# Optimization experiments

Hardware: AMD Instinct MI355X
Metric: run time of the kernel (lower is better)

## Reference

```python
import jax, jax.numpy as jnp
import numpy as np

IN_DIM, HIDDEN, OUT_DIM, BRANCH = 700, 1024, 20, 4
B, T = 128, 250
VTH = 1.0
WARMUP = 0
# surrogate-gradient constants (DH-SNN ActFun_adp); only used in backward
GAMMA, LENS, SCALE, HIGHT = 0.5, 0.5, 6.0, 0.15
SQRT2PI = float(np.sqrt(2.0 * np.pi))


def _gauss(x, mu, sigma):
    return jnp.exp(-((x - mu) ** 2) / (2.0 * sigma * sigma)) / (SQRT2PI * sigma)


@jax.custom_vjp
def spike_fn(x):
    # heaviside spike with multi-gaussian surrogate gradient
    return (x > 0).astype(x.dtype)


def _spike_fwd(x):
    return spike_fn(x), x


def _spike_bwd(x, g):
    temp = (_gauss(x, 0.0, LENS) * (1.0 + HIGHT)
            - _gauss(x, LENS, SCALE * LENS) * HIGHT
            - _gauss(x, -LENS, SCALE * LENS) * HIGHT)
    return (g * temp * GAMMA,)


spike_fn.defvjp(_spike_fwd, _spike_bwd)


def _branch_mask(rng):
    # each neuron's branch j sees a random disjoint slice of the (input+recurrent) fan-in
    isz = IN_DIM + HIDDEN
    seg = isz // BRANCH
    mask = np.zeros((HIDDEN * BRANCH, isz), np.float32)
    for i in range(HIDDEN):
        perm = rng.permutation(isz)
        for j in range(BRANCH):
            mask[i * BRANCH + j, perm[j * seg:(j + 1) * seg]] = 1.0
    return mask


def setup_inputs() -> dict:
    key = jax.random.key(0)
    ks = jax.random.split(key, 8)
    isz = IN_DIM + HIDDEN
    x = jax.random.normal(ks[0], (B, T, IN_DIM), jnp.float32)
    W = jax.random.normal(ks[1], (HIDDEN * BRANCH, isz), jnp.float32) / np.float32(np.sqrt(isz))
    W = W * jnp.asarray(_branch_mask(np.random.RandomState(0)))  # apply_mask() pre-applied
    b = jnp.zeros((HIDDEN * BRANCH,), jnp.float32)
    tau_m = jax.random.uniform(ks[2], (HIDDEN,), jnp.float32, 0.0, 4.0)
    tau_n = jax.random.uniform(ks[3], (HIDDEN, BRANCH), jnp.float32, 2.0, 6.0)  # low_n/high_n
    Wr = jax.random.normal(ks[4], (OUT_DIM, HIDDEN), jnp.float32) / np.float32(np.sqrt(HIDDEN))
    br = jnp.zeros((OUT_DIM,), jnp.float32)
    tau_r = jax.random.uniform(ks[5], (OUT_DIM,), jnp.float32, 0.0, 4.0)
    mem0 = jax.random.uniform(ks[6], (B, HIDDEN), jnp.float32) * VTH  # set_neuron_state: rand*vth
    return {"x": x, "W": W, "b": b, "tau_m": tau_m, "tau_n": tau_n,
            "Wr": Wr, "br": br, "tau_r": tau_r, "mem0": mem0}


def reference(x, W, b, tau_m, tau_n, Wr, br, tau_r, mem0):
    Bsz, Tlen = x.shape[0], x.shape[1]
    beta = jax.nn.sigmoid(tau_n)      # [H, BR] dendritic branch decay
    alpha = jax.nn.sigmoid(tau_m)     # [H]     soma decay
    alpha_r = jax.nn.sigmoid(tau_r)   # [O]     readout decay
    spike0 = jnp.zeros((Bsz, HIDDEN), x.dtype)
    d0 = jnp.zeros((Bsz, HIDDEN, BRANCH), x.dtype)
    rmem0 = jnp.zeros((Bsz, OUT_DIM), x.dtype)
    acc0 = jnp.zeros((Bsz, OUT_DIM), x.dtype)

    def step(carry, inp):
        mem, spk, d_in, rmem, acc = carry
        x_t, t = inp
        k = jnp.concatenate([x_t, spk], axis=1)                 # [B, in+H]
        cur = (k @ W.T + b).reshape(Bsz, HIDDEN, BRANCH)        # branch currents
        d_in = beta * d_in + (1.0 - beta) * cur                 # dendritic integration
        l_in = d_in.sum(axis=2)                                 # [B, H]
        mem = mem * alpha + (1.0 - alpha) * l_in - VTH * spk    # soma, soft reset (R_m=1)
        spk = spike_fn(mem - VTH)
        rmem = rmem * alpha_r + (1.0 - alpha_r) * (spk @ Wr.T + br)
        acc = acc + jnp.where(t > WARMUP, jax.nn.softmax(rmem, axis=1), 0.0)
        return (mem, spk, d_in, rmem, acc), None

    xs = (jnp.swapaxes(x, 0, 1), jnp.arange(Tlen))
    (_, _, _, _, acc), _ = jax.lax.scan(step, (mem0, spike0, d0, rmem0, acc0), xs)
    return acc
```

## Files before the change

### kernel.cpp

```cpp
#include <hip/hip_runtime.h>
#include <hip/hip_bf16.h>
#include <stdint.h>


typedef short short8 __attribute__((ext_vector_type(8)));
typedef float f32x4 __attribute__((ext_vector_type(4)));

#define T_STEPS 250
#define BATCH   128
#define HID     1024
#define NCOL    4096
#define IND     700
#define ISZ     1724
#define KPAD    704
#define OUTD    20
#define WGT     256
#define UPB     5632

#define O_P1F   0
#define O_SUM   4096
#define O_CHK   8192
#define O_WST   73728
#define O_WXH   16850944
#define O_XH    22618112

#define SM_BP    0
#define SM_A2    45568
#define SM_CURL2 135680
#define SM_MTB   144896
#define SM_TOTAL 153600

#define AGENT __HIP_MEMORY_SCOPE_AGENT

__device__ __forceinline__ float sigmoidf(float x) { return 1.0f / (1.0f + expf(-x)); }

__device__ __forceinline__ unsigned ldsLd(const unsigned* p) {
    return __hip_atomic_load(p, __ATOMIC_ACQUIRE, __HIP_MEMORY_SCOPE_WORKGROUP);
}
__device__ __forceinline__ void ldsSt(unsigned* p, unsigned v) {
    __hip_atomic_store(p, v, __ATOMIC_RELEASE, __HIP_MEMORY_SCOPE_WORKGROUP);
}

__device__ __forceinline__ void dma16(const void* g, void* l) {
    __builtin_amdgcn_global_load_lds(
        (const __attribute__((address_space(1))) unsigned int*)g,
        (__attribute__((address_space(3))) unsigned int*)l, 16, 0, 0);
}

__device__ __forceinline__ float qsum4(float v) {
    union { float f; int i; } a, b;
    a.f = v; b.i = __builtin_amdgcn_mov_dpp(a.i, 0xB1, 0xF, 0xF, true); v += b.f;
    a.f = v; b.i = __builtin_amdgcn_mov_dpp(a.i, 0x4E, 0xF, 0xF, true); v += b.f;
    return v;
}

__global__ void prep_x(const float* __restrict__ x, __hip_bfloat16* __restrict__ Xh) {
    const int total = T_STEPS * 2 * UPB;
    for (int unit = blockIdx.x * blockDim.x + threadIdx.x; unit < total;
         unit += gridDim.x * blockDim.x) {
        int q   = unit % UPB;
        int blk = unit / UPB;
        int half = blk & 1, t = blk >> 1;
        int row = q / 88, m = q % 88;
        int k8  = m ^ (row & 7);
        int b   = half * 64 + row;
        const float* xp = x + ((long)b * T_STEPS + t) * IND + k8 * 8;
        short8 o;
        #pragma unroll
        for (int e = 0; e < 8; ++e) {
            int k = k8 * 8 + e;
            float v = (k < IND) ? xp[e] : 0.0f;
            union { __hip_bfloat16 h; short s; } u;
            u.h = __float2bfloat16(v);
            o[e] = u.s;
        }
        *(short8*)(Xh + (size_t)unit * 8) = o;
    }
}

__global__ void prep_w(const float* __restrict__ W, __hip_bfloat16* __restrict__ Wxh,
                       uint64_t* __restrict__ p1f, uint64_t* __restrict__ sums,
                       uint64_t* __restrict__ chunks) {
    if (blockIdx.x == 0) {
        for (int i = threadIdx.x; i < 512; i += blockDim.x)
            __hip_atomic_store(&p1f[i], 0ull, __ATOMIC_RELAXED, AGENT);
        for (int i = threadIdx.x; i < 2 * 2 * 128; i += blockDim.x)
            __hip_atomic_store(&sums[i], 0ull, __ATOMIC_RELAXED, AGENT);
        for (int i = threadIdx.x; i < 2 * 2 * 128 * 16; i += blockDim.x)
            __hip_atomic_store(&chunks[i], 0ull, __ATOMIC_RELAXED, AGENT);
    }
    const int total = NCOL * KPAD;
    for (int idx = blockIdx.x * blockDim.x + threadIdx.x; idx < total; idx += gridDim.x * blockDim.x) {
        int k = idx % KPAD;
        int n = idx / KPAD;
        float v = (k < IND) ? W[(long)n * ISZ + k] : 0.0f;
        Wxh[idx] = __float2bfloat16(v);
    }
}

__global__ __launch_bounds__(256) void prep_t(const float* __restrict__ W, float* __restrict__ Wst) {
    __shared__ float tile[32][33];
    const int h0 = blockIdx.x * 32, n0 = blockIdx.y * 32;
    const int tx = threadIdx.x, ty = threadIdx.y;
    #pragma unroll
    for (int j = 0; j < 32; j += 8)
        tile[ty + j][tx] = W[(long)(n0 + ty + j) * ISZ + IND + h0 + tx];
    __syncthreads();
    #pragma unroll
    for (int j = 0; j < 32; j += 8)
        Wst[(long)(h0 + ty + j) * NCOL + n0 + tx] = tile[tx][ty + j];
}

__global__ __launch_bounds__(256, 2) void p1_scan(
    const __hip_bfloat16* __restrict__ Xh, const __hip_bfloat16* __restrict__ Wxh,
    const float* __restrict__ bvec, const float* __restrict__ tau_m,
    const float* __restrict__ tau_n, const float* __restrict__ mem0,
    uint64_t* __restrict__ p1f)
{
    __shared__ __align__(16) uint8_t Abuf[3 * 22528];
    __shared__ __align__(16) float preg[8 * 256];
    __shared__ unsigned anySpkF;

    const int wg    = blockIdx.x;
    const int rtile = wg & 7;
    const int ctile = wg >> 3;
    const int tid   = threadIdx.x;
    const int lane  = tid & 63, wid = tid >> 6;
    const int colA  = lane & 15, kb8 = (lane >> 4) * 8;
    const int cg    = wid >> 1;
    const int p     = wid & 1;

    if (tid == 0) anySpkF = 0u;

    const int colG0 = ctile * 64 + cg * 32 + colA;
    const int colG1 = colG0 + 16;
    const int rowB  = rtile * 16 + (lane >> 4) * 4;
    float bt_[2], omb_[2], bias_[2], al_[2], oma_[2], dn[2][4], mem_[2][4];
    {
        const int cG[2] = {colG0, colG1};
        #pragma unroll
        for (int i = 0; i < 2; ++i) {
            bt_[i]   = sigmoidf(tau_n[cG[i]]);
            omb_[i]  = 1.0f - bt_[i];
            bias_[i] = bvec[cG[i]];
            al_[i]   = sigmoidf(tau_m[cG[i] >> 2]);
            oma_[i]  = 1.0f - al_[i];
            #pragma unroll
            for (int j = 0; j < 4; ++j) {
                dn[i][j]   = 0.0f;
                mem_[i][j] = mem0[(rowB + j) * HID + (cG[i] >> 2)];
            }
        }
    }

    short8 Breg[22];
    #pragma unroll
    for (int j = 0; j < 11; ++j) {
        Breg[2 * j]     = *(const short8*)(Wxh + (long)colG0 * KPAD + (11 * p + j) * 32 + kb8);
        Breg[2 * j + 1] = *(const short8*)(Wxh + (long)colG1 * KPAD + (11 * p + j) * 32 + kb8);
    }
    asm volatile("s_waitcnt vmcnt(0)" ::: "memory");
    __builtin_amdgcn_sched_barrier(0);
    #pragma unroll
    for (int i = 0; i < 22; ++i) asm volatile("" : "+v"(Breg[i]));

    const size_t sliceBase = (size_t)(rtile >> 2) * 90112 + (size_t)(rtile & 3) * 22528;
    const int dstart = (wid < 2) ? wid * 6 : 12 + (wid - 2) * 5;
    const int dcnt   = (wid < 2) ? 6 : 5;
    const char* XhB  = (const char*)Xh;

    #pragma unroll
    for (int i = 0; i < 6; ++i)
        if (i < dcnt)
            dma16(XhB + sliceBase + (size_t)(dstart + i) * 1024 + (size_t)lane * 16,
                  Abuf + (dstart + i) * 1024);
    #pragma unroll
    for (int i = 0; i < 6; ++i)
        if (i < dcnt)
            dma16(XhB + sliceBase + 180224 + (size_t)(dstart + i) * 1024 + (size_t)lane * 16,
                  Abuf + 22528 + (dstart + i) * 1024);
    asm volatile("s_waitcnt vmcnt(5)" ::: "memory");
    __builtin_amdgcn_sched_barrier(0);
    __syncthreads();

    float memmax = -1e30f;
    const int rl = lane & 15;
    const int sw = rl & 7;
    for (int t = 0; t < T_STEPS; ++t) {
        if (t + 2 < T_STEPS) {
            const char* g = XhB + sliceBase + (size_t)(t + 2) * 180224;
            uint8_t* d = Abuf + ((t + 2) % 3) * 22528;
            #pragma unroll
            for (int i = 0; i < 6; ++i)
                if (i < dcnt)
                    dma16(g + (size_t)(dstart + i) * 1024 + (size_t)lane * 16,
                          d + (dstart + i) * 1024);
        }

        f32x4 acc0 = {0,0,0,0}, acc1 = {0,0,0,0};
        const uint8_t* Ab = Abuf + (t % 3) * 22528;
        #pragma unroll
        for (int j = 0; j < 11; ++j) {
            int k8 = (11 * p + j) * 4 + (lane >> 4);
            short8 a = *(const short8*)(Ab + ((rl * 88 + (k8 ^ sw)) << 4));
            acc0 = __builtin_amdgcn_mfma_f32_16x16x32_bf16(a, Breg[2 * j],     acc0, 0, 0, 0);
            acc1 = __builtin_amdgcn_mfma_f32_16x16x32_bf16(a, Breg[2 * j + 1], acc1, 0, 0, 0);
        }

        {
            float* w0 = preg + ((cg * 2 + (1 - p)) * 2 + 0) * 256 + lane * 4;
            *(f32x4*)w0         = acc0;
            *(f32x4*)(w0 + 256) = acc1;
        }
        asm volatile("s_waitcnt vmcnt(5) lgkmcnt(0)" ::: "memory");
        __builtin_amdgcn_sched_barrier(0);
        __builtin_amdgcn_s_barrier();

        f32x4 cs0, cs1;
        {
            const float* r0 = preg + ((cg * 2 + p) * 2 + 0) * 256 + lane * 4;
            cs0 = acc0 + *(const f32x4*)r0;
            cs1 = acc1 + *(const f32x4*)(r0 + 256);
        }
        #pragma unroll
        for (int j = 0; j < 4; ++j) {
            float d0 = bt_[0] * dn[0][j] + omb_[0] * (cs0[j] + bias_[0]);
            float d1 = bt_[1] * dn[1][j] + omb_[1] * (cs1[j] + bias_[1]);
            dn[0][j] = d0; dn[1][j] = d1;
            float l0 = qsum4(d0), l1 = qsum4(d1);
            float m0 = al_[0] * mem_[0][j] + oma_[0] * l0;
            float m1 = al_[1] * mem_[1][j] + oma_[1] * l1;
            mem_[0][j] = m0; mem_[1][j] = m1;
            memmax = fmaxf(memmax, fmaxf(m0, m1));
        }
        asm volatile("s_waitcnt lgkmcnt(0)" ::: "memory");
        __builtin_amdgcn_sched_barrier(0);
        __builtin_amdgcn_s_barrier();
    }

    if (__any(memmax > 1.0f) && lane == 0) anySpkF = 1u;
    __syncthreads();
    if (tid == 0)
        __hip_atomic_store(p1f + wg, (1ull << 32) | (uint64_t)anySpkF,
                           __ATOMIC_RELAXED, AGENT);
}

__global__ __launch_bounds__(256, 1) void p2_fallback(
    const __hip_bfloat16* __restrict__ Xh, const __hip_bfloat16* __restrict__ Wxh,
    const float* __restrict__ Wst, const uint64_t* __restrict__ p1f,
    uint64_t* __restrict__ sums, uint64_t* __restrict__ chunks,
    const float* __restrict__ bvec, const float* __restrict__ tau_m, const float* __restrict__ tau_n,
    const float* __restrict__ Wr, const float* __restrict__ brv, const float* __restrict__ tau_r,
    const float* __restrict__ mem0, float* __restrict__ out)
{
    __shared__ __align__(16) char smem[SM_TOTAL];
    __shared__ uint32_t stageW[16];
    __shared__ uint64_t roSnap[16];
    __shared__ unsigned fPollDone[2], fStgw[2], fCorr[2];
    __shared__ unsigned fRoSnap, dirtyH[2];

    __hip_bfloat16* Bp    = (__hip_bfloat16*)(smem + SM_BP);
    uint8_t*        Apre2 = (uint8_t*)(smem + SM_A2);
    float*          curL2 = (float*)(smem + SM_CURL2);
    uint8_t*        mTb   = (uint8_t*)(smem + SM_MTB);

    const int wg   = blockIdx.x;
    const int tid  = threadIdx.x;
    const int lane = tid & 63, wid = tid >> 6;
    const int colA = lane & 15, kb8 = (lane >> 4) * 8;

    if (tid < 2) { fPollDone[tid] = 0; fStgw[tid] = 0; fCorr[tid] = 0; dirtyH[tid] = 0; }
    if (tid == 0) fRoSnap = 0;
    __syncthreads();

    {
        uint64_t v0 = p1f[tid];
        uint64_t v1 = p1f[tid + 256];
        if ((unsigned)v0) dirtyH[(tid & 7) >> 2] = 1u;
        if ((unsigned)v1) dirtyH[((tid + 256) & 7) >> 2] = 1u;
    }
    __syncthreads();

    float r_alpha = 0.f, r_bias = 0.f;
    const float* WrRow = Wr;
    if (wid == 0 && lane < 32) {
        int o = (lane < OUTD) ? lane : 0;
        r_alpha = sigmoidf(tau_r[o]);
        r_bias  = brv[o];
        WrRow   = Wr + o * HID;
    }

    if (wg < BATCH && wid == 0 && lane < 32 && !dirtyH[wg >> 6]) {
        float rr = 0.f, racc = 0.f;
        for (int t = 0; t < T_STEPS; ++t) {
            rr = r_alpha * rr + (1.0f - r_alpha) * r_bias;
            float vmax = (lane < OUTD) ? rr : -__builtin_inff();
            #pragma unroll
            for (int d = 16; d > 0; d >>= 1) vmax = fmaxf(vmax, __shfl_xor(vmax, d, 32));
            float e = (lane < OUTD) ? expf(rr - vmax) : 0.f;
            float ss = e;
            #pragma unroll
            for (int d = 16; d > 0; d >>= 1) ss += __shfl_xor(ss, d, 32);
            if (t >= 1) racc += e / ss;
        }
        if (lane < OUTD) out[wg * OUTD + lane] = racc;
    }
    if (!dirtyH[wg >> 7]) return;

    float r_rmem = 0.f, r_acc = 0.f;
    const int w2    = wg & 127;
    const int bhalf = wg >> 7;
    const int bbase = bhalf * 64;
    const int c0    = w2 * 32;
    const int i0    = w2 * 8;
    const int roB2  = (wg < 64) ? wg : ((wg >= 128 && wg < 192) ? wg - 64 : -1);

    for (int idx = tid; idx < 32 * 88; idx += WGT) {
        int col = idx / 88, m = idx % 88;
        *(short8*)(Bp + col * 712 + m * 8) = *(const short8*)(Wxh + (long)(c0 + col) * KPAD + m * 8);
    }
    for (int idx = tid; idx < 64 * 136 / 4; idx += WGT)
        ((uint32_t*)mTb)[idx] = 0u;

    const int mwid = wid - 2;
    const int st   = tid - 128;
    const int r2   = st >> 1;
    const int half = st & 1;
    float dn2[16], bt2[16], omb2[16], bias2[16], alph2[4], oma2[4], mem2[4], spk2[4];
    if (wid >= 2) {
        const int b2 = bbase + r2;
        #pragma unroll
        for (int n = 0; n < 4; ++n) {
            int i = i0 + half * 4 + n;
            alph2[n] = sigmoidf(tau_m[i]);
            oma2[n]  = 1.0f - alph2[n];
            mem2[n]  = mem0[b2 * HID + i];
            spk2[n]  = 0.0f;
            #pragma unroll
            for (int j = 0; j < 4; ++j) {
                int idx = n * 4 + j;
                bt2[idx]   = sigmoidf(tau_n[i * 4 + j]);
                omb2[idx]  = 1.0f - bt2[idx];
                bias2[idx] = bvec[i * 4 + j];
                dn2[idx]   = 0.0f;
            }
        }
    }
    const int trRow = mwid * 32;
    const int rb2   = trRow + (lane & 15);
    const int sw2   = rb2 & 7;
    uint8_t* dst2   = Apre2 + mwid * 45056;

    if (wid >= 2) {
        const char* gsrc = (const char*)Xh + ((size_t)bhalf * UPB) * 16 + (size_t)mwid * 45056;
        #pragma unroll
        for (int i = 0; i < 44; ++i)
            dma16(gsrc + i * 1024 + lane * 16, dst2 + i * 1024);
    }
    asm volatile("s_waitcnt vmcnt(0)" ::: "memory");
    __syncthreads();

    if (wid < 2) {
        const int plane = tid;
        for (int k = 1; k <= T_STEPS; ++k) {
            const size_t base = ((size_t)((k - 1) & 1) * 2 + bhalf) * 128 + plane;
            const unsigned want = (unsigned)(k + 1);
            uint64_t v;
            for (;;) {
                v = __hip_atomic_load(sums + base, __ATOMIC_RELAXED, AGENT);
                if ((unsigned)(v >> 32) == want) break;
                __builtin_amdgcn_s_sleep(1);
            }
            unsigned mysum = (unsigned)v;
            if (mysum) {
                if (wid == 1)
                    while (ldsLd(&fRoSnap) < (unsigned)(k - 1)) {}
                const uint64_t* rec = chunks + base * 16;
                uint8_t* col = mTb + plane;
                unsigned pend = mysum;
                while (pend) {
                    int c = __builtin_ctz(pend);
                    uint64_t cv = __hip_atomic_load(rec + c, __ATOMIC_RELAXED, AGENT);
                    if ((unsigned)(cv >> 32) == want) {
                        pend &= pend - 1;
                        unsigned pay = (unsigned)cv;
                        col[(4 * c + 0) * 136] = (uint8_t)(pay);
                        col[(4 * c + 1) * 136] = (uint8_t)(pay >> 8);
                        col[(4 * c + 2) * 136] = (uint8_t)(pay >> 16);
                        col[(4 * c + 3) * 136] = (uint8_t)(pay >> 24);
                    } else {
                        __builtin_amdgcn_s_sleep(1);
                    }
                }
            }
            const bool anyW = __any(mysum != 0u);
            if (lane == 0)
                ldsSt(&fPollDone[wid], ((unsigned)k << 1) | (anyW ? 1u : 0u));

            if (wid == 0) {
                while ((ldsLd(&fPollDone[1]) >> 1) < (unsigned)k) {}
                if (roB2 >= 0 && lane < 16)
                    roSnap[lane] = ((const uint64_t*)(mTb + (roB2 & 63) * 136))[lane];
                asm volatile("s_waitcnt lgkmcnt(0)" ::: "memory");
                if (lane == 0) ldsSt(&fRoSnap, (unsigned)k);
                if (roB2 >= 0 && lane < 32) {
                    float rsum = 0.f;
                    #pragma unroll 4
                    for (int q = 0; q < 16; ++q) {
                        uint64_t mword = roSnap[q];
                        while (mword) {
                            int h = (q << 6) + __builtin_ctzll(mword);
                            mword &= mword - 1;
                            rsum += WrRow[h];
                        }
                    }
                    r_rmem = r_alpha * r_rmem + (1.0f - r_alpha) * (rsum + r_bias);
                    float vmax = (lane < OUTD) ? r_rmem : -__builtin_inff();
                    #pragma unroll
                    for (int d = 16; d > 0; d >>= 1) vmax = fmaxf(vmax, __shfl_xor(vmax, d, 32));
                    float e = (lane < OUTD) ? expf(r_rmem - vmax) : 0.f;
                    float ssum = e;
                    #pragma unroll
                    for (int d = 16; d > 0; d >>= 1) ssum += __shfl_xor(ssum, d, 32);
                    if (k >= 2) r_acc += e / ssum;
                }
            }
        }
        if (wid == 0 && roB2 >= 0 && lane < OUTD) out[roB2 * OUTD + lane] = r_acc;
    } else {
        const float* clp = curL2 + r2 * 36 + half * 16;
        for (int t = 0; t < T_STEPS; ++t) {
            f32x4 a00 = {0,0,0,0}, a01 = {0,0,0,0}, a10 = {0,0,0,0}, a11 = {0,0,0,0};
            #pragma unroll
            for (int k0 = 0; k0 < KPAD; k0 += 32) {
                int k8 = (k0 >> 3) + (lane >> 4);
                short8 f0 = *(const short8*)&Apre2[(((rb2)      * 88 + (k8 ^ sw2)) << 4)];
                short8 f1 = *(const short8*)&Apre2[(((rb2 + 16) * 88 + (k8 ^ sw2)) << 4)];
                short8 b0 = *(const short8*)(&Bp[(colA) * 712 + k0 + kb8]);
                short8 b1 = *(const short8*)(&Bp[(16 + colA) * 712 + k0 + kb8]);
                a00 = __builtin_amdgcn_mfma_f32_16x16x32_bf16(f0, b0, a00, 0, 0, 0);
                a01 = __builtin_amdgcn_mfma_f32_16x16x32_bf16(f0, b1, a01, 0, 0, 0);
                a10 = __builtin_amdgcn_mfma_f32_16x16x32_bf16(f1, b0, a10, 0, 0, 0);
                a11 = __builtin_amdgcn_mfma_f32_16x16x32_bf16(f1, b1, a11, 0, 0, 0);
            }
            asm volatile("s_waitcnt lgkmcnt(0)" ::: "memory");
            __builtin_amdgcn_sched_barrier(0);
            if (t + 1 < T_STEPS) {
                const char* gsrc = (const char*)Xh
                    + (((size_t)(t + 1) * 2 + bhalf) * UPB) * 16 + (size_t)mwid * 45056;
                #pragma unroll
                for (int i = 0; i < 44; ++i)
                    dma16(gsrc + i * 1024 + lane * 16, dst2 + i * 1024);
            }
            {
                const int crow0 = trRow + ((lane >> 4) << 2);
                #pragma unroll
                for (int j = 0; j < 4; ++j) {
                    curL2[(crow0 + j) * 36 + colA]           = a00[j];
                    curL2[(crow0 + j) * 36 + 16 + colA]      = a01[j];
                    curL2[(crow0 + 16 + j) * 36 + colA]      = a10[j];
                    curL2[(crow0 + 16 + j) * 36 + 16 + colA] = a11[j];
                }
            }
            asm volatile("s_waitcnt lgkmcnt(0)" ::: "memory");
            __builtin_amdgcn_sched_barrier(0);

            f32x4 cv0 = *(const f32x4*)(clp + 0);
            f32x4 cv1 = *(const f32x4*)(clp + 4);
            f32x4 cv2 = *(const f32x4*)(clp + 8);
            f32x4 cv3 = *(const f32x4*)(clp + 12);
            float cl[16];
            #pragma unroll
            for (int e = 0; e < 4; ++e) {
                cl[e] = cv0[e]; cl[4 + e] = cv1[e]; cl[8 + e] = cv2[e]; cl[12 + e] = cv3[e];
            }
            float memS[4], spkS[4];
            #pragma unroll
            for (int n = 0; n < 4; ++n) {
                float lin = 0.f;
                #pragma unroll
                for (int j = 0; j < 4; ++j) {
                    int idx = n * 4 + j;
                    dn2[idx] = bt2[idx] * dn2[idx] + omb2[idx] * (cl[idx] + bias2[idx]);
                    lin += dn2[idx];
                }
                memS[n] = alph2[n] * mem2[n] + oma2[n] * lin - spk2[n];
                spkS[n] = (memS[n] > 1.0f) ? 1.0f : 0.0f;
            }
            unsigned nib = 0;
            #pragma unroll
            for (int n = 0; n < 4; ++n) nib |= (spkS[n] != 0.f ? 1u : 0u) << (half * 4 + n);
            nib |= (unsigned)__shfl_xor((int)nib, 1);
            if (half == 0) ((uint8_t*)stageW)[r2] = (uint8_t)nib;
            if (lane == 0) ldsSt(&fStgw[mwid], (unsigned)(t + 1));

            bool anySpk = false;
            if (t > 0) {
                unsigned p0, p1;
                do { p0 = ldsLd(&fPollDone[0]); } while ((p0 >> 1) < (unsigned)t);
                do { p1 = ldsLd(&fPollDone[1]); } while ((p1 >> 1) < (unsigned)t);
                anySpk = ((p0 | p1) & 1u) != 0u;
            }
            if (anySpk) {
                float recv[16];
                #pragma unroll
                for (int e = 0; e < 16; ++e) recv[e] = 0.f;
                const float* Wb = Wst + c0 + half * 16;
                const uint64_t* mrow = (const uint64_t*)(mTb + r2 * 136);
                for (int q = 0; q < 16; ++q) {
                    uint64_t mword = mrow[q];
                    while (mword) {
                        int h = (q << 6) + __builtin_ctzll(mword);
                        mword &= mword - 1;
                        const f32x4* wv = (const f32x4*)(Wb + (long)h * NCOL);
                        f32x4 w0 = wv[0], w1 = wv[1], w2v = wv[2], w3 = wv[3];
                        #pragma unroll
                        for (int e = 0; e < 4; ++e) {
                            recv[e] += w0[e]; recv[4 + e] += w1[e];
                            recv[8 + e] += w2v[e]; recv[12 + e] += w3[e];
                        }
                    }
                }
                #pragma unroll
                for (int n = 0; n < 4; ++n) {
                    float cs = 0.f;
                    #pragma unroll
                    for (int j = 0; j < 4; ++j) {
                        int idx = n * 4 + j;
                        float ad = omb2[idx] * recv[idx];
                        dn2[idx] += ad; cs += ad;
                    }
                    memS[n] += oma2[n] * cs;
                    spkS[n] = (memS[n] > 1.0f) ? 1.0f : 0.0f;
                }
                unsigned nib2 = 0;
                #pragma unroll
                for (int n = 0; n < 4; ++n) nib2 |= (spkS[n] != 0.f ? 1u : 0u) << (half * 4 + n);
                nib2 |= (unsigned)__shfl_xor((int)nib2, 1);
                if (half == 0) ((uint8_t*)stageW)[r2] = (uint8_t)nib2;
                if (roB2 >= 0) while (ldsLd(&fRoSnap) < (unsigned)t) {}
                uint64_t* mz = (uint64_t*)(mTb + r2 * 136) + half * 8;
                #pragma unroll
                for (int e = 0; e < 8; ++e) mz[e] = 0;
                if (lane == 0) ldsSt(&fCorr[mwid], (unsigned)(t + 1));
            }
            #pragma unroll
            for (int n = 0; n < 4; ++n) { mem2[n] = memS[n]; spk2[n] = spkS[n]; }

            if (mwid == 0) {
                while (ldsLd(&fStgw[1]) < (unsigned)(t + 1)) {}
                if (anySpk) while (ldsLd(&fCorr[1]) < (unsigned)(t + 1)) {}
                unsigned pay = (lane < 16) ? stageW[lane] : 0u;
                const size_t pbase = ((size_t)(t & 1) * 2 + bhalf) * 128 + w2;
                if (lane < 16 && pay)
                    __hip_atomic_store(chunks + pbase * 16 + lane,
                                       ((uint64_t)(unsigned)(t + 2) << 32) | (uint64_t)pay,
                                       __ATOMIC_RELAXED, AGENT);
                uint64_t bal = __ballot(pay != 0u);
                if (lane == 0)
                    __hip_atomic_store(sums + pbase,
                                       ((uint64_t)(unsigned)(t + 2) << 32) | (uint64_t)(bal & 0xFFFFull),
                                       __ATOMIC_RELAXED, AGENT);
            }
            asm volatile("s_waitcnt vmcnt(0)" ::: "memory");
        }
    }
}

extern "C" void kernel_launch(void* const* d_in, const int* in_sizes, int n_in,
                              void* d_out, int out_size, void* d_ws, size_t ws_size,
                              hipStream_t stream) {
    (void)in_sizes; (void)n_in; (void)out_size; (void)ws_size;
    const float* x     = (const float*)d_in[0];
    const float* W     = (const float*)d_in[1];
    const float* bv    = (const float*)d_in[2];
    const float* tau_m = (const float*)d_in[3];
    const float* tau_n = (const float*)d_in[4];
    const float* Wr    = (const float*)d_in[5];
    const float* br    = (const float*)d_in[6];
    const float* tau_r = (const float*)d_in[7];
    const float* mem0  = (const float*)d_in[8];

    char* ws = (char*)d_ws;
    uint64_t*        p1flag = (uint64_t*)(ws + O_P1F);
    uint64_t*        sums   = (uint64_t*)(ws + O_SUM);
    uint64_t*        chunks = (uint64_t*)(ws + O_CHK);
    float*           Wst    = (float*)(ws + O_WST);
    __hip_bfloat16*  Wxh    = (__hip_bfloat16*)(ws + O_WXH);
    __hip_bfloat16*  Xh     = (__hip_bfloat16*)(ws + O_XH);

    prep_x<<<2048, 256, 0, stream>>>(x, Xh);
    prep_w<<<2048, 256, 0, stream>>>(W, Wxh, p1flag, sums, chunks);
    dim3 g3(32, 128), b3(32, 8);
    prep_t<<<g3, b3, 0, stream>>>(W, Wst);
    p1_scan<<<512, WGT, 0, stream>>>(Xh, Wxh, bv, tau_m, tau_n, mem0, p1flag);
    p2_fallback<<<256, WGT, 0, stream>>>(Xh, Wxh, Wst, p1flag, sums, chunks,
                                         bv, tau_m, tau_n, Wr, br, tau_r, mem0, (float*)d_out);
}
```

Before: 452.1 us.

## Fuse prep kernels and software-pipeline the p1 scan update behind MFMAs

Merges the three preprocessing kernels into one launch and vectorizes the fp32 loads for x and W. In p1_scan the per-step barriers drop from two to one: preg is double-buffered and each step's neuron update runs on the previous step's sums while the current MFMAs execute. The A-tile prefetch goes from triple to double buffering with a full vmcnt(0) wait each step, which may expose more global-load latency. This trades prefetch depth for fewer barriers and more overlap of MFMA and VALU work.

```diff
diff --git a/kernel.cpp b/kernel.cpp
--- a/kernel.cpp
+++ b/kernel.cpp
@@ -54,61 +54,85 @@
     return v;
 }
 
-__global__ void prep_x(const float* __restrict__ x, __hip_bfloat16* __restrict__ Xh) {
-    const int total = T_STEPS * 2 * UPB;
-    for (int unit = blockIdx.x * blockDim.x + threadIdx.x; unit < total;
-         unit += gridDim.x * blockDim.x) {
-        int q   = unit % UPB;
-        int blk = unit / UPB;
-        int half = blk & 1, t = blk >> 1;
-        int row = q / 88, m = q % 88;
-        int k8  = m ^ (row & 7);
-        int b   = half * 64 + row;
-        const float* xp = x + ((long)b * T_STEPS + t) * IND + k8 * 8;
-        short8 o;
+__device__ __forceinline__ short bf16bits(float v) {
+    union { __hip_bfloat16 h; short s; } u;
+    u.h = __float2bfloat16(v);
+    return u.s;
+}
+
+__global__ __launch_bounds__(256) void prep_all(
+    const float* __restrict__ x, const float* __restrict__ W,
+    __hip_bfloat16* __restrict__ Xh, __hip_bfloat16* __restrict__ Wxh,
+    float* __restrict__ Wst, uint64_t* __restrict__ p1f,
+    uint64_t* __restrict__ sums, uint64_t* __restrict__ chunks)
+{
+    const int bid = blockIdx.x;
+    const int tid = threadIdx.x;
+
+    if (bid < 2048) {
+        const int total = T_STEPS * 2 * UPB;
+        for (int unit = bid * 256 + tid; unit < total; unit += 2048 * 256) {
+            int q    = unit % UPB;
+            int blk  = unit / UPB;
+            int half = blk & 1, t = blk >> 1;
+            int row  = q / 88, m = q % 88;
+            int k8   = m ^ (row & 7);
+            int b    = half * 64 + row;
+            int k0   = k8 * 8;
+            const float* xp = x + ((long)b * T_STEPS + t) * IND + k0;
+            short8 o;
+            if (k0 + 8 <= IND) {
+                f32x4 v0 = *(const f32x4*)xp;
+                f32x4 v1 = *(const f32x4*)(xp + 4);
+                #pragma unroll
+                for (int e = 0; e < 4; ++e) { o[e] = bf16bits(v0[e]); o[4 + e] = bf16bits(v1[e]); }
+            } else {
+                #pragma unroll
+                for (int e = 0; e < 8; ++e)
+                    o[e] = bf16bits((k0 + e < IND) ? xp[e] : 0.0f);
+            }
+            *(short8*)(Xh + (size_t)unit * 8) = o;
+        }
+    } else if (bid < 4096) {
+        if (bid == 2048) {
+            for (int i = tid; i < 512; i += 256)
+                __hip_atomic_store(&p1f[i], 0ull, __ATOMIC_RELAXED, AGENT);
+            for (int i = tid; i < 2 * 2 * 128; i += 256)
+                __hip_atomic_store(&sums[i], 0ull, __ATOMIC_RELAXED, AGENT);
+            for (int i = tid; i < 2 * 2 * 128 * 16; i += 256)
+                __hip_atomic_store(&chunks[i], 0ull, __ATOMIC_RELAXED, AGENT);
+        }
+        const int total = NCOL * 88;
+        for (int unit = (bid - 2048) * 256 + tid; unit < total; unit += 2048 * 256) {
+            int n = unit / 88, m = unit % 88;
+            int k0 = m * 8;
+            const float* wp = W + (long)n * ISZ + k0;
+            short8 o;
+            if (k0 + 8 <= IND) {
+                f32x4 v0 = *(const f32x4*)wp;
+                f32x4 v1 = *(const f32x4*)(wp + 4);
+                #pragma unroll
+                for (int e = 0; e < 4; ++e) { o[e] = bf16bits(v0[e]); o[4 + e] = bf16bits(v1[e]); }
+            } else {
+                #pragma unroll
+                for (int e = 0; e < 8; ++e)
+                    o[e] = bf16bits((k0 + e < IND) ? wp[e] : 0.0f);
+            }
+            *(short8*)(Wxh + (long)n * KPAD + k0) = o;
+        }
+    } else {
+        __shared__ float tile[32][33];
+        const int idx = bid - 4096;
+        const int h0 = (idx & 31) * 32, n0 = (idx >> 5) * 32;
+        const int tx = tid & 31, ty = tid >> 5;
         #pragma unroll
-        for (int e = 0; e < 8; ++e) {
-            int k = k8 * 8 + e;
-            float v = (k < IND) ? xp[e] : 0.0f;
-            union { __hip_bfloat16 h; short s; } u;
-            u.h = __float2bfloat16(v);
-            o[e] = u.s;
-        }
-        *(short8*)(Xh + (size_t)unit * 8) = o;
-    }
-}
-
-__global__ void prep_w(const float* __restrict__ W, __hip_bfloat16* __restrict__ Wxh,
-                       uint64_t* __restrict__ p1f, uint64_t* __restrict__ sums,
-                       uint64_t* __restrict__ chunks) {
-    if (blockIdx.x == 0) {
-        for (int i = threadIdx.x; i < 512; i += blockDim.x)
-            __hip_atomic_store(&p1f[i], 0ull, __ATOMIC_RELAXED, AGENT);
-        for (int i = threadIdx.x; i < 2 * 2 * 128; i += blockDim.x)
-            __hip_atomic_store(&sums[i], 0ull, __ATOMIC_RELAXED, AGENT);
-        for (int i = threadIdx.x; i < 2 * 2 * 128 * 16; i += blockDim.x)
-            __hip_atomic_store(&chunks[i], 0ull, __ATOMIC_RELAXED, AGENT);
-    }
-    const int total = NCOL * KPAD;
-    for (int idx = blockIdx.x * blockDim.x + threadIdx.x; idx < total; idx += gridDim.x * blockDim.x) {
-        int k = idx % KPAD;
-        int n = idx / KPAD;
-        float v = (k < IND) ? W[(long)n * ISZ + k] : 0.0f;
-        Wxh[idx] = __float2bfloat16(v);
-    }
-}
-
-__global__ __launch_bounds__(256) void prep_t(const float* __restrict__ W, float* __restrict__ Wst) {
-    __shared__ float tile[32][33];
-    const int h0 = blockIdx.x * 32, n0 = blockIdx.y * 32;
-    const int tx = threadIdx.x, ty = threadIdx.y;
-    #pragma unroll
-    for (int j = 0; j < 32; j += 8)
-        tile[ty + j][tx] = W[(long)(n0 + ty + j) * ISZ + IND + h0 + tx];
-    __syncthreads();
-    #pragma unroll
-    for (int j = 0; j < 32; j += 8)
-        Wst[(long)(h0 + ty + j) * NCOL + n0 + tx] = tile[tx][ty + j];
+        for (int j = 0; j < 32; j += 8)
+            tile[ty + j][tx] = W[(long)(n0 + ty + j) * ISZ + IND + h0 + tx];
+        __syncthreads();
+        #pragma unroll
+        for (int j = 0; j < 32; j += 8)
+            Wst[(long)(h0 + ty + j) * NCOL + n0 + tx] = tile[tx][ty + j];
+    }
 }
 
 __global__ __launch_bounds__(256, 2) void p1_scan(
@@ -117,8 +141,8 @@
     const float* __restrict__ tau_n, const float* __restrict__ mem0,
     uint64_t* __restrict__ p1f)
 {
-    __shared__ __align__(16) uint8_t Abuf[3 * 22528];
-    __shared__ __align__(16) float preg[8 * 256];
+    __shared__ __align__(16) uint8_t Abuf[2][22528];
+    __shared__ __align__(16) float preg[2][8 * 256];
     __shared__ unsigned anySpkF;
 
     const int wg    = blockIdx.x;
@@ -169,73 +193,93 @@
     const int dcnt   = (wid < 2) ? 6 : 5;
     const char* XhB  = (const char*)Xh;
 
-    #pragma unroll
-    for (int i = 0; i < 6; ++i)
-        if (i < dcnt)
-            dma16(XhB + sliceBase + (size_t)(dstart + i) * 1024 + (size_t)lane * 16,
-                  Abuf + (dstart + i) * 1024);
-    #pragma unroll
-    for (int i = 0; i < 6; ++i)
-        if (i < dcnt)
-            dma16(XhB + sliceBase + 180224 + (size_t)(dstart + i) * 1024 + (size_t)lane * 16,
-                  Abuf + 22528 + (dstart + i) * 1024);
-    asm volatile("s_waitcnt vmcnt(5)" ::: "memory");
+    #define ISSUE_A(T, BUF)                                                            \
+        do {                                                                           \
+            const char* _g = XhB + sliceBase + (size_t)(T) * 180224;                   \
+            _Pragma("unroll")                                                          \
+            for (int _i = 0; _i < 6; ++_i)                                             \
+                if (_i < dcnt)                                                         \
+                    dma16(_g + (size_t)(dstart + _i) * 1024 + (size_t)lane * 16,       \
+                          (BUF) + (dstart + _i) * 1024);                               \
+        } while (0)
+
+    const int rl = lane & 15;
+    const int sw = rl & 7;
+
+    #define MFMA_BLOCK(AB, A0, A1)                                                             \
+        do {                                                                                   \
+            _Pragma("unroll")                                                                  \
+            for (int _j = 0; _j < 11; ++_j) {                                                  \
+                int _k8 = (11 * p + _j) * 4 + (lane >> 4);                                     \
+                short8 _a = *(const short8*)((AB) + ((rl * 88 + (_k8 ^ sw)) << 4));            \
+                A0 = __builtin_amdgcn_mfma_f32_16x16x32_bf16(_a, Breg[2 * _j],     A0, 0,0,0); \
+                A1 = __builtin_amdgcn_mfma_f32_16x16x32_bf16(_a, Breg[2 * _j + 1], A1, 0,0,0); \
+            }                                                                                  \
+        } while (0)
+
+    #define UPDATE_STEP(CS0, CS1)                                                  \
+        do {                                                                       \
+            _Pragma("unroll")                                                      \
+            for (int _j = 0; _j < 4; ++_j) {                                       \
+                float _d0 = bt_[0] * dn[0][_j] + omb_[0] * ((CS0)[_j] + bias_[0]); \
+                float _d1 = bt_[1] * dn[1][_j] + omb_[1] * ((CS1)[_j] + bias_[1]); \
+                dn[0][_j] = _d0; dn[1][_j] = _d1;                                  \
+                float _l0 = qsum4(_d0), _l1 = qsum4(_d1);                          \
+                float _m0 = al_[0] * mem_[0][_j] + oma_[0] * _l0;                  \
+                float _m1 = al_[1] * mem_[1][_j] + oma_[1] * _l1;                  \
+                mem_[0][_j] = _m0; mem_[1][_j] = _m1;                              \
+                memmax = fmaxf(memmax, fmaxf(_m0, _m1));                           \
+            }                                                                      \
+        } while (0)
+
+    float memmax = -1e30f;
+    f32x4 own0, own1, prt0, prt1;
+    const int wrSlot = (cg * 2 + (1 - p)) * 2;
+    const int rdSlot = (cg * 2 + p) * 2;
+
+    ISSUE_A(0, Abuf[0]);
+    asm volatile("s_waitcnt vmcnt(0)" ::: "memory");
     __builtin_amdgcn_sched_barrier(0);
     __syncthreads();
 
-    float memmax = -1e30f;
-    const int rl = lane & 15;
-    const int sw = rl & 7;
-    for (int t = 0; t < T_STEPS; ++t) {
-        if (t + 2 < T_STEPS) {
-            const char* g = XhB + sliceBase + (size_t)(t + 2) * 180224;
-            uint8_t* d = Abuf + ((t + 2) % 3) * 22528;
-            #pragma unroll
-            for (int i = 0; i < 6; ++i)
-                if (i < dcnt)
-                    dma16(g + (size_t)(dstart + i) * 1024 + (size_t)lane * 16,
-                          d + (dstart + i) * 1024);
-        }
-
+    {
+        ISSUE_A(1, Abuf[1]);
         f32x4 acc0 = {0,0,0,0}, acc1 = {0,0,0,0};
-        const uint8_t* Ab = Abuf + (t % 3) * 22528;
-        #pragma unroll
-        for (int j = 0; j < 11; ++j) {
-            int k8 = (11 * p + j) * 4 + (lane >> 4);
-            short8 a = *(const short8*)(Ab + ((rl * 88 + (k8 ^ sw)) << 4));
-            acc0 = __builtin_amdgcn_mfma_f32_16x16x32_bf16(a, Breg[2 * j],     acc0, 0, 0, 0);
-            acc1 = __builtin_amdgcn_mfma_f32_16x16x32_bf16(a, Breg[2 * j + 1], acc1, 0, 0, 0);
-        }
-
-        {
-            float* w0 = preg + ((cg * 2 + (1 - p)) * 2 + 0) * 256 + lane * 4;
-            *(f32x4*)w0         = acc0;
-            *(f32x4*)(w0 + 256) = acc1;
-        }
-        asm volatile("s_waitcnt vmcnt(5) lgkmcnt(0)" ::: "memory");
+        MFMA_BLOCK(Abuf[0], acc0, acc1);
+        float* wq = &preg[0][wrSlot * 256 + lane * 4];
+        *(f32x4*)wq = acc0; *(f32x4*)(wq + 256) = acc1;
+        asm volatile("s_waitcnt vmcnt(0) lgkmcnt(0)" ::: "memory");
         __builtin_amdgcn_sched_barrier(0);
         __builtin_amdgcn_s_barrier();
-
-        f32x4 cs0, cs1;
+        const float* rq = &preg[0][rdSlot * 256 + lane * 4];
+        prt0 = *(const f32x4*)rq; prt1 = *(const f32x4*)(rq + 256);
+        own0 = acc0; own1 = acc1;
+    }
+
+    for (int t = 1; t < T_STEPS; ++t) {
+        if (t + 1 < T_STEPS)
+            ISSUE_A(t + 1, Abuf[(t + 1) & 1]);
+        f32x4 acc0 = {0,0,0,0}, acc1 = {0,0,0,0};
+        MFMA_BLOCK(Abuf[t & 1], acc0, acc1);
         {
-            const float* r0 = preg + ((cg * 2 + p) * 2 + 0) * 256 + lane * 4;
-            cs0 = acc0 + *(const f32x4*)r0;
-            cs1 = acc1 + *(const f32x4*)(r0 + 256);
-        }
-        #pragma unroll
-        for (int j = 0; j < 4; ++j) {
-            float d0 = bt_[0] * dn[0][j] + omb_[0] * (cs0[j] + bias_[0]);
-            float d1 = bt_[1] * dn[1][j] + omb_[1] * (cs1[j] + bias_[1]);
-            dn[0][j] = d0; dn[1][j] = d1;
-            float l0 = qsum4(d0), l1 = qsum4(d1);
-            float m0 = al_[0] * mem_[0][j] + oma_[0] * l0;
-            float m1 = al_[1] * mem_[1][j] + oma_[1] * l1;
-            mem_[0][j] = m0; mem_[1][j] = m1;
-            memmax = fmaxf(memmax, fmaxf(m0, m1));
-        }
-        asm volatile("s_waitcnt lgkmcnt(0)" ::: "memory");
+            f32x4 cs0 = own0 + prt0;
+            f32x4 cs1 = own1 + prt1;
+            UPDATE_STEP(cs0, cs1);
+        }
+        float* wq = &preg[t & 1][wrSlot * 256 + lane * 4];
+        *(f32x4*)wq = acc0; *(f32x4*)(wq + 256) = acc1;
+        asm volatile("s_waitcnt vmcnt(0) lgkmcnt(0)" ::: "memory");
         __builtin_amdgcn_sched_barrier(0);
         __builtin_amdgcn_s_barrier();
+        const float* rq = &preg[t & 1][rdSlot * 256 + lane * 4];
+        prt0 = *(const f32x4*)rq; prt1 = *(const f32x4*)(rq + 256);
+        own0 = acc0; own1 = acc1;
+    }
+
+    {
+        f32x4 cs0 = own0 + prt0;
+        f32x4 cs1 = own1 + prt1;
+        UPDATE_STEP(cs0, cs1);
     }
 
     if (__any(memmax > 1.0f) && lane == 0) anySpkF = 1u;
@@ -243,6 +287,9 @@
     if (tid == 0)
         __hip_atomic_store(p1f + wg, (1ull << 32) | (uint64_t)anySpkF,
                            __ATOMIC_RELAXED, AGENT);
+    #undef ISSUE_A
+    #undef MFMA_BLOCK
+    #undef UPDATE_STEP
 }
 
 __global__ __launch_bounds__(256, 1) void p2_fallback(
@@ -589,10 +636,7 @@
     __hip_bfloat16*  Wxh    = (__hip_bfloat16*)(ws + O_WXH);
     __hip_bfloat16*  Xh     = (__hip_bfloat16*)(ws + O_XH);
 
-    prep_x<<<2048, 256, 0, stream>>>(x, Xh);
-    prep_w<<<2048, 256, 0, stream>>>(W, Wxh, p1flag, sums, chunks);
-    dim3 g3(32, 128), b3(32, 8);
-    prep_t<<<g3, b3, 0, stream>>>(W, Wst);
+    prep_all<<<8192, 256, 0, stream>>>(x, W, Xh, Wxh, Wst, p1flag, sums, chunks);
     p1_scan<<<512, WGT, 0, stream>>>(Xh, Wxh, bv, tau_m, tau_n, mem0, p1flag);
     p2_fallback<<<256, WGT, 0, stream>>>(Xh, Wxh, Wst, p1flag, sums, chunks,
                                          bv, tau_m, tau_n, Wr, br, tau_r, mem0, (float*)d_out);
```

New measurement: 385.0 us. -14.8%, faster.
